# Performance work log

Hardware: AMD Instinct MI355X
Metric: run time of the kernel (lower is better)

The kernel has to match this reference:

```python
import jax, jax.numpy as jnp
import numpy as np

K = 2.0          # arctan surrogate sharpness (init kwarg k)
THRESHOLD = 1.0  # init kwarg threshold


def _binop(ei, ej):
    # linear recurrence combine: (A, Bu) pairs, v_t = A_t*v_{t-1} + Bu_t
    a_i, b_i = ei
    a_j, b_j = ej
    return a_j * a_i, a_j * b_i + b_j


def _pscan(tau, x):
    # x: [B, T, H]; tau: [H] broadcast over batch and time (matches
    # jnp.repeat(tau[None], T, 0) inside vmap over batch in the original).
    tau_b = jnp.broadcast_to(tau, x.shape)
    _, v = jax.lax.associative_scan(_binop, (tau_b, x), axis=1)
    return v


@jax.custom_vjp
def _spike(x):
    # spyx arctan surrogate: forward is Heaviside, backward 1/(1+(k*x)^2)
    return jnp.where(x > 0, 1.0, 0.0).astype(x.dtype)


def _spike_fwd(x):
    return _spike(x), x


def _spike_bwd(x, g):
    return (g / (1.0 + (K * x) ** 2),)


_spike.defvjp(_spike_fwd, _spike_bwd)


def setup_inputs() -> dict:
    key = jax.random.key(0)
    k1, k2 = jax.random.split(key)
    x = jax.random.normal(k1, (16, 1024, 1024), dtype=jnp.float32)
    # beta ~ TruncatedNormal(mean=0.25, std=0.5), as in hk.initializers
    beta = 0.25 + 0.5 * jax.random.truncated_normal(k2, -2.0, 2.0, (1024,), jnp.float32)
    return {"x": x, "beta": beta}


def reference(x, beta):
    b = jnp.clip(beta, 0.0, 1.0)
    V = _pscan(b, x)                      # membrane potential scan
    R = _pscan(b, jax.nn.sigmoid(V))      # refractory/reset scan
    return _spike(V - R - THRESHOLD), V
```

## Files before the change

### kernel.cpp

```cpp
#include <hip/hip_runtime.h>


#define BB 16
#define TT 1024
#define HH 1024
#define L 32
#define C 32
#define SEQ 32

__global__ __launch_bounds__(1024, 4) void lif_scan(const float* __restrict__ x,
                                                    const float* __restrict__ beta,
                                                    float* __restrict__ out_spike,
                                                    float* __restrict__ out_v) {
    __shared__ float lds_v[C][SEQ];
    __shared__ float lds_r[C][SEQ];

    const int tid = threadIdx.x;
    const int c = tid >> 5;
    const int s = tid & 31;
    const int blk = blockIdx.x;
    const int b = blk >> 5;
    const int h = ((blk & 31) << 5) + s;

    const float bf = fminf(fmaxf(beta[h], 0.0f), 1.0f);
    float pwL = bf;
#pragma unroll
    for (int k = 0; k < 5; ++k) pwL *= pwL;

    const size_t base = (size_t)b * TT * HH + (size_t)(c * L) * HH + (size_t)h;
    const float* __restrict__ xp = x + base;
    float* __restrict__ vp = out_v + base;
    float* __restrict__ sp = out_spike + base;

    float arr[L];
#pragma unroll
    for (int i = 0; i < L; ++i) arr[i] = xp[(size_t)i * HH];

    float V = 0.0f;
#pragma unroll
    for (int i = 0; i < L; ++i) {
        V = fmaf(bf, V, arr[i]);
        arr[i] = V;
    }
    lds_v[c][s] = V;
    __syncthreads();

    float Vstart = 0.0f;
    for (int j = 0; j < c; ++j) Vstart = fmaf(pwL, Vstart, lds_v[j][s]);

    float vcarry = Vstart;
    float R = 0.0f;
#pragma unroll
    for (int i = 0; i < L; ++i) {
        vcarry *= bf;
        const float vfull = arr[i] + vcarry;
        vp[(size_t)i * HH] = vfull;
        const float sg = 1.0f / (1.0f + __expf(-vfull));
        R = fmaf(bf, R, sg);
        arr[i] = vfull - R;
    }
    lds_r[c][s] = R;
    __syncthreads();

    float Rstart = 0.0f;
    for (int j = 0; j < c; ++j) Rstart = fmaf(pwL, Rstart, lds_r[j][s]);

    float rcarry = Rstart;
#pragma unroll
    for (int i = 0; i < L; ++i) {
        rcarry *= bf;
        sp[(size_t)i * HH] = (arr[i] - rcarry > 1.0f) ? 1.0f : 0.0f;
    }
}

extern "C" void kernel_launch(void* const* d_in, const int* in_sizes, int n_in,
                              void* d_out, int out_size, void* d_ws, size_t ws_size,
                              hipStream_t stream) {
    const float* x = (const float*)d_in[0];
    const float* beta = (const float*)d_in[1];
    float* out = (float*)d_out;
    float* out_spike = out;
    float* out_v = out + (size_t)BB * TT * HH;

    const int grid = (BB * HH) / SEQ;
    lif_scan<<<grid, 1024, 0, stream>>>(x, beta, out_spike, out_v);
}
```

Measured before the change: 190.1 us.

## Vectorize LIF scan to float4 per thread with 64 time chunks

Each thread now handles four adjacent hidden channels as float4 and a 16-step time chunk, with 64 chunks per block of 512 threads. Loads and stores become 128-bit accesses with nontemporal hints, and the sigmoid uses a fast reciprocal intrinsic. The aim is fewer memory instructions and less cache pollution on a bandwidth-bound scan. In exchange, the serial carry combine over chunk totals runs up to 64 steps, and the approximate reciprocal can flip spikes that sit near the threshold.

```diff
diff --git a/kernel.cpp b/kernel.cpp
--- a/kernel.cpp
+++ b/kernel.cpp
@@ -4,72 +4,89 @@
 #define BB 16
 #define TT 1024
 #define HH 1024
-#define L 32
-#define C 32
-#define SEQ 32
+#define L 16
+#define C 64
+#define G 8
 
-__global__ __launch_bounds__(1024, 4) void lif_scan(const float* __restrict__ x,
-                                                    const float* __restrict__ beta,
-                                                    float* __restrict__ out_spike,
-                                                    float* __restrict__ out_v) {
-    __shared__ float lds_v[C][SEQ];
-    __shared__ float lds_r[C][SEQ];
+typedef float f4 __attribute__((ext_vector_type(4)));
+
+__device__ __forceinline__ f4 fma4(f4 a, f4 b, f4 c) {
+    f4 r;
+#pragma unroll
+    for (int k = 0; k < 4; ++k) r[k] = fmaf(a[k], b[k], c[k]);
+    return r;
+}
+
+__global__ __launch_bounds__(512, 4) void lif_scan(const float* __restrict__ x,
+                                                   const float* __restrict__ beta,
+                                                   float* __restrict__ out_spike,
+                                                   float* __restrict__ out_v) {
+    __shared__ f4 lds_v[C][G];
+    __shared__ f4 lds_r[C][G];
 
     const int tid = threadIdx.x;
-    const int c = tid >> 5;
-    const int s = tid & 31;
+    const int g = tid & (G - 1);
+    const int c = tid >> 3;
     const int blk = blockIdx.x;
     const int b = blk >> 5;
-    const int h = ((blk & 31) << 5) + s;
+    const int h0 = ((blk & 31) << 5) + (g << 2);
 
-    const float bf = fminf(fmaxf(beta[h], 0.0f), 1.0f);
-    float pwL = bf;
+    f4 bf = *reinterpret_cast<const f4*>(beta + h0);
 #pragma unroll
-    for (int k = 0; k < 5; ++k) pwL *= pwL;
+    for (int k = 0; k < 4; ++k) bf[k] = fminf(fmaxf(bf[k], 0.0f), 1.0f);
+    f4 pw = bf;
+#pragma unroll
+    for (int k = 0; k < 4; ++k) pw *= pw;
 
-    const size_t base = (size_t)b * TT * HH + (size_t)(c * L) * HH + (size_t)h;
-    const float* __restrict__ xp = x + base;
-    float* __restrict__ vp = out_v + base;
-    float* __restrict__ sp = out_spike + base;
+    const size_t base = (size_t)b * TT * HH + (size_t)(c * L) * HH + (size_t)h0;
+    const f4* __restrict__ xv = reinterpret_cast<const f4*>(x + base);
+    f4* __restrict__ vv = reinterpret_cast<f4*>(out_v + base);
+    f4* __restrict__ sv = reinterpret_cast<f4*>(out_spike + base);
+    const int STRD = HH / 4;
 
-    float arr[L];
+    f4 arr[L];
 #pragma unroll
-    for (int i = 0; i < L; ++i) arr[i] = xp[(size_t)i * HH];
+    for (int i = 0; i < L; ++i) arr[i] = __builtin_nontemporal_load(xv + (size_t)i * STRD);
 
-    float V = 0.0f;
+    f4 V = (f4)0.0f;
 #pragma unroll
     for (int i = 0; i < L; ++i) {
-        V = fmaf(bf, V, arr[i]);
+        V = fma4(bf, V, arr[i]);
         arr[i] = V;
     }
-    lds_v[c][s] = V;
+    lds_v[c][g] = V;
     __syncthreads();
 
-    float Vstart = 0.0f;
-    for (int j = 0; j < c; ++j) Vstart = fmaf(pwL, Vstart, lds_v[j][s]);
+    f4 Vstart = (f4)0.0f;
+    for (int j = 0; j < c; ++j) Vstart = fma4(pw, Vstart, lds_v[j][g]);
 
-    float vcarry = Vstart;
-    float R = 0.0f;
+    f4 vc = Vstart;
+    f4 R = (f4)0.0f;
 #pragma unroll
     for (int i = 0; i < L; ++i) {
-        vcarry *= bf;
-        const float vfull = arr[i] + vcarry;
-        vp[(size_t)i * HH] = vfull;
-        const float sg = 1.0f / (1.0f + __expf(-vfull));
-        R = fmaf(bf, R, sg);
-        arr[i] = vfull - R;
+        vc *= bf;
+        const f4 vf = arr[i] + vc;
+        __builtin_nontemporal_store(vf, vv + (size_t)i * STRD);
+        f4 sg;
+#pragma unroll
+        for (int k = 0; k < 4; ++k) sg[k] = __builtin_amdgcn_rcpf(1.0f + __expf(-vf[k]));
+        R = fma4(bf, R, sg);
+        arr[i] = vf - R;
     }
-    lds_r[c][s] = R;
+    lds_r[c][g] = R;
     __syncthreads();
 
-    float Rstart = 0.0f;
-    for (int j = 0; j < c; ++j) Rstart = fmaf(pwL, Rstart, lds_r[j][s]);
+    f4 Rstart = (f4)0.0f;
+    for (int j = 0; j < c; ++j) Rstart = fma4(pw, Rstart, lds_r[j][g]);
 
-    float rcarry = Rstart;
+    f4 rc = Rstart;
 #pragma unroll
     for (int i = 0; i < L; ++i) {
-        rcarry *= bf;
-        sp[(size_t)i * HH] = (arr[i] - rcarry > 1.0f) ? 1.0f : 0.0f;
+        rc *= bf;
+        f4 sp;
+#pragma unroll
+        for (int k = 0; k < 4; ++k) sp[k] = (arr[i][k] - rc[k] > 1.0f) ? 1.0f : 0.0f;
+        __builtin_nontemporal_store(sp, sv + (size_t)i * STRD);
     }
 }
 
@@ -82,6 +99,6 @@
     float* out_spike = out;
     float* out_v = out + (size_t)BB * TT * HH;
 
-    const int grid = (BB * HH) / SEQ;
-    lif_scan<<<grid, 1024, 0, stream>>>(x, beta, out_spike, out_v);
+    const int grid = (BB * HH) / 32;
+    lif_scan<<<grid, 512, 0, stream>>>(x, beta, out_spike, out_v);
 }
```

After: 200.5 us. 5.5% more time.
